# Kernel optimization log

Hardware: AMD Instinct MI355X
Metric: run time of the kernel (lower is better)

The kernel has to match this reference:

```python
import jax, jax.numpy as jnp
import numpy as np
from jax import lax

C, K, G = 256, 3, 8
CG = C // G          # group channels
P = K * K            # sampling points per group
STRIDE, PAD, DIL = 1, 1, 1
OFFSET_SCALE = 1.0
EPS = 1e-5


def setup_inputs() -> dict:
    key = jax.random.key(0)
    ks = jax.random.split(key, 8)
    N, H, W = 4, 64, 64
    return {
        "x": jax.random.normal(ks[0], (N, C, H, W), jnp.float32),
        "dw_w": jax.random.normal(ks[1], (C, 1, K, K), jnp.float32) * 0.1,
        "dw_b": jax.random.normal(ks[2], (C,), jnp.float32) * 0.01,
        "gn_g": jnp.ones((C,), jnp.float32),
        "gn_b": jnp.zeros((C,), jnp.float32),
        "off_w": jax.random.normal(ks[3], (C, G * P * 2), jnp.float32) * 0.01,
        "off_b": jax.random.normal(ks[4], (G * P * 2,), jnp.float32) * 0.1,
        "mask_w": jax.random.normal(ks[5], (C, G * P), jnp.float32) * 0.02,
        "mask_b": jax.random.normal(ks[6], (G * P,), jnp.float32) * 0.02,
    }


def _dcnv3_core(x_nhwc, offset, mask):
    # x_nhwc (N,H,W,C); offset (N,Ho,Wo,G*P*2); mask (N,Ho,Wo,G*P) already softmaxed
    inp = jnp.pad(x_nhwc, ((0, 0), (PAD, PAD), (PAD, PAD), (0, 0)))
    N, Hp, Wp, _ = inp.shape
    Ho = (Hp - (DIL * (K - 1) + 1)) // STRIDE + 1
    Wo = (Wp - (DIL * (K - 1) + 1)) // STRIDE + 1
    base = (DIL * (K - 1)) // 2 + 0.5
    ref_y = (base + jnp.arange(Ho, dtype=jnp.float32) * STRIDE) / Hp  # (Ho,)
    ref_x = (base + jnp.arange(Wo, dtype=jnp.float32) * STRIDE) / Wp  # (Wo,)
    # dilation grid; flatten order p = iw*K + ih (matches torch meshgrid(x,y) ij)
    kvals = jnp.arange(K, dtype=jnp.float32) * DIL - (DIL * (K - 1)) // 2
    gx = jnp.repeat(kvals, K) / Wp  # (P,)
    gy = jnp.tile(kvals, K) / Hp    # (P,)
    off = offset.reshape(N, Ho, Wo, G, P, 2)
    # normalized sampling locations in [0,1] (then grid_sample convention 2*loc-1)
    loc_x = ref_x[None, None, :, None, None] + gx * OFFSET_SCALE + off[..., 0] * OFFSET_SCALE / Wp
    loc_y = ref_y[None, :, None, None, None] + gy * OFFSET_SCALE + off[..., 1] * OFFSET_SCALE / Hp
    # pixel coords, align_corners=False: px = loc*size - 0.5
    px = loc_x * Wp - 0.5
    py = loc_y * Hp - 0.5
    x0 = jnp.floor(px)
    y0 = jnp.floor(py)
    wx = px - x0
    wy = py - y0
    x0i = x0.astype(jnp.int32)
    y0i = y0.astype(jnp.int32)

    inp_flat = inp.reshape(N, Hp * Wp, G, CG)
    n_idx = jnp.arange(N)[:, None, None, None, None]
    g_idx = jnp.arange(G)[None, None, None, :, None]

    def gather(yi, xi):
        # zeros padding: clamp index, zero out-of-bounds corners
        valid = (yi >= 0) & (yi < Hp) & (xi >= 0) & (xi < Wp)
        idx = jnp.clip(yi, 0, Hp - 1) * Wp + jnp.clip(xi, 0, Wp - 1)
        v = inp_flat[n_idx, idx, g_idx]  # (N,Ho,Wo,G,P,CG)
        return v * valid[..., None]

    m = mask.reshape(N, Ho, Wo, G, P)
    out = jnp.zeros((N, Ho, Wo, G, CG), jnp.float32)
    for dy, dx, w in ((0, 0, (1 - wy) * (1 - wx)), (0, 1, (1 - wy) * wx),
                      (1, 0, wy * (1 - wx)), (1, 1, wy * wx)):
        v = gather(y0i + dy, x0i + dx)
        out = out + jnp.einsum('nhwgp,nhwgpc->nhwgc', m * w, v)
    return out.reshape(N, Ho, Wo, G * CG)


def reference(x, dw_w, dw_b, gn_g, gn_b, off_w, off_b, mask_w, mask_b):
    N, _, H, W = x.shape
    # depthwise 3x3 conv (groups=channels)
    x1 = lax.conv_general_dilated(
        x, dw_w, (1, 1), [((K - 1) // 2, (K - 1) // 2)] * 2,
        dimension_numbers=('NCHW', 'OIHW', 'NCHW'), feature_group_count=C)
    x1 = x1 + dw_b[None, :, None, None]
    # GroupNorm with num_groups=1: normalize over (C,H,W) per sample
    mu = jnp.mean(x1, axis=(1, 2, 3), keepdims=True)
    var = jnp.mean((x1 - mu) ** 2, axis=(1, 2, 3), keepdims=True)
    x1 = (x1 - mu) * lax.rsqrt(var + EPS)
    x1 = x1 * gn_g[None, :, None, None] + gn_b[None, :, None, None]
    x1 = jax.nn.gelu(x1, approximate=False)
    x1 = jnp.transpose(x1, (0, 2, 3, 1))  # NHWC
    offset = x1 @ off_w + off_b                                  # (N,H,W,G*P*2)
    mask = jax.nn.softmax((x1 @ mask_w + mask_b).reshape(N, H, W, G, P), axis=-1)
    mask = mask.reshape(N, H, W, G * P)
    out = _dcnv3_core(jnp.transpose(x, (0, 2, 3, 1)), offset, mask)
    return jnp.transpose(out, (0, 3, 1, 2))  # back to NCHW
```

## Files before the change

### kernel.cpp

```cpp
#include <hip/hip_runtime.h>
#include <math.h>

#define NB   4
#define CH   256
#define HW   4096
#define NCOL 216
#define MTOT 16384
#define CHW  1048576
#define EPSV 1e-5f

#define OFF_NHWC 0
#define NHWCSZ   (NB*HW*CH/2)
#define OFF_OM   (OFF_NHWC + NHWCSZ)
#define OMSZ     (MTOT*NCOL/2)
#define OFF_AB   (OFF_OM + OMSZ)
#define ABSZ     (MTOT*CH/2)
#define OFF_WB   (OFF_AB + ABSZ)
#define WBSZ     (CH*CH/2)
#define OFF_BI   (OFF_WB + WBSZ)
#define OFF_PT   (OFF_BI + 256)

typedef short bf16x8 __attribute__((ext_vector_type(8)));
typedef float f32x4  __attribute__((ext_vector_type(4)));

__device__ __forceinline__ unsigned short f2bf(float f) {
    unsigned int u = __builtin_bit_cast(unsigned int, f);
    u += 0x7fffu + ((u >> 16) & 1u);
    return (unsigned short)(u >> 16);
}

__device__ __forceinline__ float bf2f(unsigned short s) {
    return __builtin_bit_cast(float, (unsigned int)s << 16);
}

__global__ __launch_bounds__(256) void conv_prep_kernel(
    const float* __restrict__ x, const float* __restrict__ dw_w,
    const float* __restrict__ dw_b,
    const float* __restrict__ off_w, const float* __restrict__ off_b,
    const float* __restrict__ mask_w, const float* __restrict__ mask_b,
    unsigned short* __restrict__ A, unsigned short* __restrict__ inp_nhwc,
    unsigned short* __restrict__ Wc_bt, float* __restrict__ bias,
    float* __restrict__ partials) {
    __shared__ float xs[32 * 108];
    __shared__ unsigned short tb[32 * 36];
    __shared__ float rs1[256], rs2[256];
    int b = blockIdx.x;
    int tid = threadIdx.x;
    if (b < 256) {
        int k = b, n = tid;
        float v = 0.f;
        if (n < 144)      v = off_w[k * 144 + n];
        else if (n < 216) v = mask_w[k * 72 + (n - 144)];
        Wc_bt[(size_t)n * 256 + k] = f2bf(v);
        if (b == 0) {
            float bb = 0.f;
            if (n < 144)      bb = off_b[n];
            else if (n < 216) bb = mask_b[n - 144];
            bias[n] = bb;
        }
    }
    int ct  = b & 7;
    int hwt = (b >> 3) & 127;
    int n   = b >> 10;
    int c0 = ct * 32;
    int hw0 = hwt * 32;
    int h  = hw0 >> 6;
    int w0 = hw0 & 63;
    const float* xb = x + ((size_t)n * CH + c0) * HW;
    for (int it = 0; it < 13; ++it) {
        int q = it * 256 + tid;
        if (q < 3264) {
            int cl = q / 102;
            int rr = q - cl * 102;
            int r  = rr / 34;
            int i  = rr - r * 34;
            int gh = h - 1 + r;
            int gw = w0 - 1 + i;
            float v = 0.f;
            if (gh >= 0 && gh < 64 && gw >= 0 && gw < 64)
                v = xb[(size_t)cl * HW + gh * 64 + gw];
            xs[cl * 108 + r * 36 + i] = v;
        }
    }
    __syncthreads();
    int wl = tid & 31;
    int cbase = (tid >> 5) * 4;
    float s1 = 0.f, s2 = 0.f;
    ushort4 o;
    unsigned short ov[4];
#pragma unroll
    for (int j = 0; j < 4; ++j) {
        int c = c0 + cbase + j;
        float acc = dw_b[c];
        const float* wk = dw_w + c * 9;
#pragma unroll
        for (int r = 0; r < 3; ++r)
#pragma unroll
            for (int kx = 0; kx < 3; ++kx)
                acc = fmaf(xs[(cbase + j) * 108 + r * 36 + wl + kx], wk[r * 3 + kx], acc);
        s1 += acc; s2 += acc * acc;
        ov[j] = f2bf(acc);
    }
    o.x = ov[0]; o.y = ov[1]; o.z = ov[2]; o.w = ov[3];
    *(ushort4*)&tb[wl * 36 + cbase] = o;
    rs1[tid] = s1; rs2[tid] = s2;
    {
        int r2 = tid >> 3, cg = tid & 7;
        ushort4 rv;
        rv.x = f2bf(xs[(cg * 4 + 0) * 108 + 36 + r2 + 1]);
        rv.y = f2bf(xs[(cg * 4 + 1) * 108 + 36 + r2 + 1]);
        rv.z = f2bf(xs[(cg * 4 + 2) * 108 + 36 + r2 + 1]);
        rv.w = f2bf(xs[(cg * 4 + 3) * 108 + 36 + r2 + 1]);
        *(ushort4*)&inp_nhwc[((size_t)(n * HW + hw0 + r2)) * 256 + c0 + cg * 4] = rv;
    }
    __syncthreads();
    for (int s = 128; s > 0; s >>= 1) {
        if (tid < s) { rs1[tid] += rs1[tid + s]; rs2[tid] += rs2[tid + s]; }
        __syncthreads();
    }
    if (tid == 0) {
        partials[2 * b]     = rs1[0];
        partials[2 * b + 1] = rs2[0];
    }
    int r2 = tid >> 3, cg = tid & 7;
    ushort4 w4 = *(const ushort4*)&tb[r2 * 36 + cg * 4];
    *(ushort4*)&A[((size_t)(n * HW + hw0 + r2)) * 256 + c0 + cg * 4] = w4;
}

#define LDK 72
__global__ __launch_bounds__(512) void fused_gemm_dcn_kernel(
    const unsigned short* __restrict__ A, const unsigned short* __restrict__ Bt,
    const float* __restrict__ bias, const float* __restrict__ partials,
    const float* __restrict__ gn_g, const float* __restrict__ gn_b,
    const unsigned short* __restrict__ inp_nhwc, float* __restrict__ out) {
    __shared__ unsigned short As[64 * LDK];
    __shared__ unsigned short Bs[256 * LDK];
    __shared__ float lom[64 * 216];
    __shared__ float ot[16 * 260];
    __shared__ float red1[512], red2[512];

    int bid = blockIdx.x;
    int tile = (bid & 7) * 32 + (bid >> 3);
    int m0 = tile * 64;
    int n = m0 >> 12;
    int hwb = m0 & 4095;
    int tid = threadIdx.x, lane = tid & 63, wid = tid >> 6;

    {
        const float2* p2 = (const float2*)partials;
        float2 a = p2[n * 1024 + tid];
        float2 c = p2[n * 1024 + tid + 512];
        red1[tid] = a.x + c.x;
        red2[tid] = a.y + c.y;
    }
    __syncthreads();
    for (int s = 256; s > 0; s >>= 1) {
        if (tid < s) { red1[tid] += red1[tid + s]; red2[tid] += red2[tid + s]; }
        __syncthreads();
    }
    float mean = red1[0] * (1.f / (float)CHW);
    float var  = red2[0] * (1.f / (float)CHW) - mean * mean;
    float rsig = rsqrtf(var + EPSV);

    f32x4 acc[4][2] = {};
    for (int k0 = 0; k0 < 256; k0 += 64) {
        {
            int row = tid >> 3, kk0 = (tid & 7) * 8;
            union { uint4 u; unsigned short s[8]; } in, ou;
            in.u = *(const uint4*)&A[((size_t)(m0 + row)) * 256 + k0 + kk0];
#pragma unroll
            for (int j = 0; j < 8; ++j) {
                int ch = k0 + kk0 + j;
                float v = bf2f(in.s[j]);
                v = (v - mean) * rsig * gn_g[ch] + gn_b[ch];
                v = 0.5f * v * (1.0f + erff(v * 0.70710678118654752f));
                ou.s[j] = f2bf(v);
            }
            *(uint4*)&As[row * LDK + kk0] = ou.u;
        }
#pragma unroll
        for (int i = 0; i < 4; ++i) {
            int q = i * 512 + tid;
            int mm = q >> 3, kk = (q & 7) * 8;
            *(uint4*)&Bs[mm * LDK + kk] = *(const uint4*)&Bt[(size_t)mm * 256 + k0 + kk];
        }
        __syncthreads();
#pragma unroll
        for (int kh = 0; kh < 2; ++kh) {
            bf16x8 af[4], bfr[2];
#pragma unroll
            for (int mi = 0; mi < 4; ++mi)
                af[mi] = *(const bf16x8*)&As[(mi * 16 + (lane & 15)) * LDK + kh * 32 + (lane >> 4) * 8];
#pragma unroll
            for (int nj = 0; nj < 2; ++nj)
                bfr[nj] = *(const bf16x8*)&Bs[(wid * 32 + nj * 16 + (lane & 15)) * LDK + kh * 32 + (lane >> 4) * 8];
#pragma unroll
            for (int mi = 0; mi < 4; ++mi)
#pragma unroll
                for (int nj = 0; nj < 2; ++nj)
                    acc[mi][nj] = __builtin_amdgcn_mfma_f32_16x16x32_bf16(
                        af[mi], bfr[nj], acc[mi][nj], 0, 0, 0);
        }
        __syncthreads();
    }
#pragma unroll
    for (int nj = 0; nj < 2; ++nj) {
        int col = wid * 32 + nj * 16 + (lane & 15);
        if (col < NCOL) {
            float bcol = bias[col];
#pragma unroll
            for (int mi = 0; mi < 4; ++mi)
#pragma unroll
                for (int r = 0; r < 4; ++r) {
                    int row = mi * 16 + (lane >> 4) * 4 + r;
                    lom[row * NCOL + col] = acc[mi][nj][r] + bcol;
                }
        }
    }
    __syncthreads();

    const unsigned short* base = inp_nhwc + (size_t)n * HW * 256;
    int h = hwb >> 6;
    int half = tid >> 5;
    int l  = tid & 31;
    int g  = l >> 2;
    int ch0 = l * 8;
#pragma unroll
    for (int round = 0; round < 4; ++round) {
        int pixloc = round * 16 + half;
        int w = pixloc;
        const float* lm = &lom[pixloc * NCOL];
        float lg[9];
        float mx = -1e30f;
#pragma unroll
        for (int p = 0; p < 9; ++p) { lg[p] = lm[144 + g * 9 + p]; mx = fmaxf(mx, lg[p]); }
        float sum = 0.f;
#pragma unroll
        for (int p = 0; p < 9; ++p) { lg[p] = __expf(lg[p] - mx); sum += lg[p]; }
        float rs = 1.0f / sum;
        float acc2[8] = {};
#pragma unroll
        for (int p = 0; p < 9; ++p) {
            float ox = lm[g * 18 + p * 2];
            float oy = lm[g * 18 + p * 2 + 1];
            float px = (float)(w + (p / 3)) + ox;
            float py = (float)(h + (p % 3)) + oy;
            float xf = floorf(px), yf = floorf(py);
            float wx = px - xf, wy = py - yf;
            int x0 = (int)xf, y0 = (int)yf;
            float m = lg[p] * rs;
            float w00 = m * (1.f - wy) * (1.f - wx);
            float w01 = m * (1.f - wy) * wx;
            float w10 = m * wy * (1.f - wx);
            float w11 = m * wy * wx;
#pragma unroll
            for (int corner = 0; corner < 4; ++corner) {
                int yi = y0 + (corner >> 1);
                int xi = x0 + (corner & 1);
                float cw = (corner == 0) ? w00 : (corner == 1) ? w01 : (corner == 2) ? w10 : w11;
                bool valid = (yi >= 1) & (yi <= 64) & (xi >= 1) & (xi <= 64);
                int yc = min(max(yi, 1), 64) - 1;
                int xc = min(max(xi, 1), 64) - 1;
                bf16x8 v = *(const bf16x8*)&base[((size_t)yc * 64 + xc) * 256 + ch0];
                float f = valid ? cw : 0.f;
#pragma unroll
                for (int j = 0; j < 8; ++j)
                    acc2[j] = fmaf(f, bf2f((unsigned short)v[j]), acc2[j]);
            }
        }
        *(float4*)&ot[half * 260 + ch0]     = make_float4(acc2[0], acc2[1], acc2[2], acc2[3]);
        *(float4*)&ot[half * 260 + ch0 + 4] = make_float4(acc2[4], acc2[5], acc2[6], acc2[7]);
        __syncthreads();
        int px = tid & 15, crow = tid >> 4;
#pragma unroll
        for (int cc = 0; cc < 8; ++cc) {
            int c = cc * 32 + crow;
            out[((size_t)(n * CH + c)) * HW + hwb + round * 16 + px] = ot[px * 260 + c];
        }
        __syncthreads();
    }
}

extern "C" void kernel_launch(void* const* d_in, const int* in_sizes, int n_in,
                              void* d_out, int out_size, void* d_ws, size_t ws_size,
                              hipStream_t stream) {
    const float* x      = (const float*)d_in[0];
    const float* dw_w   = (const float*)d_in[1];
    const float* dw_b   = (const float*)d_in[2];
    const float* gn_g   = (const float*)d_in[3];
    const float* gn_b   = (const float*)d_in[4];
    const float* off_w  = (const float*)d_in[5];
    const float* off_b  = (const float*)d_in[6];
    const float* mask_w = (const float*)d_in[7];
    const float* mask_b = (const float*)d_in[8];
    float* out = (float*)d_out;

    float* ws = (float*)d_ws;
    unsigned short* inp_nhwc = (unsigned short*)(ws + OFF_NHWC);
    unsigned short* Abf   = (unsigned short*)(ws + OFF_AB);
    unsigned short* Wc_bt = (unsigned short*)(ws + OFF_WB);
    float* bias     = ws + OFF_BI;
    float* partials = ws + OFF_PT;

    conv_prep_kernel<<<4096, 256, 0, stream>>>(x, dw_w, dw_b, off_w, off_b,
                                               mask_w, mask_b, Abf, inp_nhwc,
                                               Wc_bt, bias, partials);
    fused_gemm_dcn_kernel<<<256, 512, 0, stream>>>(Abf, Wc_bt, bias, partials,
                                                   gn_g, gn_b, inp_nhwc, out);
}
```

Baseline: 140.7 us.

## Vectorize halo loads, use wave-shuffle reductions, prefetch B, double-buffer output tile

Result: faster. 128.3 us (-8.8%).

```diff
diff --git a/kernel.cpp b/kernel.cpp
--- a/kernel.cpp
+++ b/kernel.cpp
@@ -41,9 +41,9 @@
     unsigned short* __restrict__ A, unsigned short* __restrict__ inp_nhwc,
     unsigned short* __restrict__ Wc_bt, float* __restrict__ bias,
     float* __restrict__ partials) {
-    __shared__ float xs[32 * 108];
+    __shared__ float xs[32 * 120];
     __shared__ unsigned short tb[32 * 36];
-    __shared__ float rs1[256], rs2[256];
+    __shared__ float rs1[4], rs2[4];
     int b = blockIdx.x;
     int tid = threadIdx.x;
     if (b < 256) {
@@ -67,20 +67,30 @@
     int h  = hw0 >> 6;
     int w0 = hw0 & 63;
     const float* xb = x + ((size_t)n * CH + c0) * HW;
-    for (int it = 0; it < 13; ++it) {
-        int q = it * 256 + tid;
-        if (q < 3264) {
-            int cl = q / 102;
-            int rr = q - cl * 102;
-            int r  = rr / 34;
-            int i  = rr - r * 34;
-            int gh = h - 1 + r;
-            int gw = w0 - 1 + i;
-            float v = 0.f;
-            if (gh >= 0 && gh < 64 && gw >= 0 && gw < 64)
-                v = xb[(size_t)cl * HW + gh * 64 + gw];
-            xs[cl * 108 + r * 36 + i] = v;
-        }
+#pragma unroll
+    for (int it = 0; it < 3; ++it) {
+        int idx = it * 256 + tid;
+        int cl  = idx / 24;
+        int rem = idx - cl * 24;
+        int r   = rem >> 3;
+        int f4  = rem & 7;
+        int gh  = h - 1 + r;
+        float4 v = make_float4(0.f, 0.f, 0.f, 0.f);
+        if (gh >= 0 && gh < 64)
+            v = *(const float4*)&xb[(size_t)cl * HW + gh * 64 + w0 + f4 * 4];
+        *(float4*)&xs[cl * 120 + r * 40 + 4 + f4 * 4] = v;
+    }
+    if (tid < 192) {
+        int cl   = tid / 6;
+        int rem  = tid - cl * 6;
+        int r    = rem >> 1;
+        int side = rem & 1;
+        int gh   = h - 1 + r;
+        int gw   = side ? (w0 + 32) : (w0 - 1);
+        float v = 0.f;
+        if (gh >= 0 && gh < 64 && gw >= 0 && gw < 64)
+            v = xb[(size_t)cl * HW + gh * 64 + gw];
+        xs[cl * 120 + r * 40 + (side ? 36 : 3)] = v;
     }
     __syncthreads();
     int wl = tid & 31;
@@ -97,30 +107,31 @@
         for (int r = 0; r < 3; ++r)
 #pragma unroll
             for (int kx = 0; kx < 3; ++kx)
-                acc = fmaf(xs[(cbase + j) * 108 + r * 36 + wl + kx], wk[r * 3 + kx], acc);
+                acc = fmaf(xs[(cbase + j) * 120 + r * 40 + wl + kx + 3], wk[r * 3 + kx], acc);
         s1 += acc; s2 += acc * acc;
         ov[j] = f2bf(acc);
     }
     o.x = ov[0]; o.y = ov[1]; o.z = ov[2]; o.w = ov[3];
     *(ushort4*)&tb[wl * 36 + cbase] = o;
-    rs1[tid] = s1; rs2[tid] = s2;
+#pragma unroll
+    for (int off = 32; off >= 1; off >>= 1) {
+        s1 += __shfl_xor(s1, off, 64);
+        s2 += __shfl_xor(s2, off, 64);
+    }
+    if ((tid & 63) == 0) { rs1[tid >> 6] = s1; rs2[tid >> 6] = s2; }
     {
         int r2 = tid >> 3, cg = tid & 7;
         ushort4 rv;
-        rv.x = f2bf(xs[(cg * 4 + 0) * 108 + 36 + r2 + 1]);
-        rv.y = f2bf(xs[(cg * 4 + 1) * 108 + 36 + r2 + 1]);
-        rv.z = f2bf(xs[(cg * 4 + 2) * 108 + 36 + r2 + 1]);
-        rv.w = f2bf(xs[(cg * 4 + 3) * 108 + 36 + r2 + 1]);
+        rv.x = f2bf(xs[(cg * 4 + 0) * 120 + 40 + r2 + 4]);
+        rv.y = f2bf(xs[(cg * 4 + 1) * 120 + 40 + r2 + 4]);
+        rv.z = f2bf(xs[(cg * 4 + 2) * 120 + 40 + r2 + 4]);
+        rv.w = f2bf(xs[(cg * 4 + 3) * 120 + 40 + r2 + 4]);
         *(ushort4*)&inp_nhwc[((size_t)(n * HW + hw0 + r2)) * 256 + c0 + cg * 4] = rv;
     }
     __syncthreads();
-    for (int s = 128; s > 0; s >>= 1) {
-        if (tid < s) { rs1[tid] += rs1[tid + s]; rs2[tid] += rs2[tid + s]; }
-        __syncthreads();
-    }
     if (tid == 0) {
-        partials[2 * b]     = rs1[0];
-        partials[2 * b + 1] = rs2[0];
+        partials[2 * b]     = rs1[0] + rs1[1] + rs1[2] + rs1[3];
+        partials[2 * b + 1] = rs2[0] + rs2[1] + rs2[2] + rs2[3];
     }
     int r2 = tid >> 3, cg = tid & 7;
     ushort4 w4 = *(const ushort4*)&tb[r2 * 36 + cg * 4];
@@ -136,8 +147,8 @@
     __shared__ unsigned short As[64 * LDK];
     __shared__ unsigned short Bs[256 * LDK];
     __shared__ float lom[64 * 216];
-    __shared__ float ot[16 * 260];
-    __shared__ float red1[512], red2[512];
+    __shared__ float ot[2 * 16 * 260];
+    __shared__ float red1[8], red2[8];
 
     int bid = blockIdx.x;
     int tile = (bid & 7) * 32 + (bid >> 3);
@@ -146,20 +157,31 @@
     int hwb = m0 & 4095;
     int tid = threadIdx.x, lane = tid & 63, wid = tid >> 6;
 
+#pragma unroll
+    for (int i = 0; i < 4; ++i) {
+        int q = i * 512 + tid;
+        int mm = q >> 3, kk = (q & 7) * 8;
+        *(uint4*)&Bs[mm * LDK + kk] = *(const uint4*)&Bt[(size_t)mm * 256 + kk];
+    }
+
     {
         const float2* p2 = (const float2*)partials;
         float2 a = p2[n * 1024 + tid];
         float2 c = p2[n * 1024 + tid + 512];
-        red1[tid] = a.x + c.x;
-        red2[tid] = a.y + c.y;
+        float s1 = a.x + c.x, s2 = a.y + c.y;
+#pragma unroll
+        for (int off = 32; off >= 1; off >>= 1) {
+            s1 += __shfl_xor(s1, off, 64);
+            s2 += __shfl_xor(s2, off, 64);
+        }
+        if (lane == 0) { red1[wid] = s1; red2[wid] = s2; }
     }
     __syncthreads();
-    for (int s = 256; s > 0; s >>= 1) {
-        if (tid < s) { red1[tid] += red1[tid + s]; red2[tid] += red2[tid + s]; }
-        __syncthreads();
-    }
-    float mean = red1[0] * (1.f / (float)CHW);
-    float var  = red2[0] * (1.f / (float)CHW) - mean * mean;
+    float t1 = 0.f, t2 = 0.f;
+#pragma unroll
+    for (int i = 0; i < 8; ++i) { t1 += red1[i]; t2 += red2[i]; }
+    float mean = t1 * (1.f / (float)CHW);
+    float var  = t2 * (1.f / (float)CHW) - mean * mean;
     float rsig = rsqrtf(var + EPSV);
 
     f32x4 acc[4][2] = {};
@@ -178,11 +200,13 @@
             }
             *(uint4*)&As[row * LDK + kk0] = ou.u;
         }
-#pragma unroll
-        for (int i = 0; i < 4; ++i) {
-            int q = i * 512 + tid;
-            int mm = q >> 3, kk = (q & 7) * 8;
-            *(uint4*)&Bs[mm * LDK + kk] = *(const uint4*)&Bt[(size_t)mm * 256 + k0 + kk];
+        if (k0) {
+#pragma unroll
+            for (int i = 0; i < 4; ++i) {
+                int q = i * 512 + tid;
+                int mm = q >> 3, kk = (q & 7) * 8;
+                *(uint4*)&Bs[mm * LDK + kk] = *(const uint4*)&Bt[(size_t)mm * 256 + k0 + kk];
+            }
         }
         __syncthreads();
 #pragma unroll
@@ -227,6 +251,7 @@
     int ch0 = l * 8;
 #pragma unroll
     for (int round = 0; round < 4; ++round) {
+        float* otb = &ot[(round & 1) * 16 * 260];
         int pixloc = round * 16 + half;
         int w = pixloc;
         const float* lm = &lom[pixloc * NCOL];
@@ -268,16 +293,15 @@
                     acc2[j] = fmaf(f, bf2f((unsigned short)v[j]), acc2[j]);
             }
         }
-        *(float4*)&ot[half * 260 + ch0]     = make_float4(acc2[0], acc2[1], acc2[2], acc2[3]);
-        *(float4*)&ot[half * 260 + ch0 + 4] = make_float4(acc2[4], acc2[5], acc2[6], acc2[7]);
+        *(float4*)&otb[half * 260 + ch0]     = make_float4(acc2[0], acc2[1], acc2[2], acc2[3]);
+        *(float4*)&otb[half * 260 + ch0 + 4] = make_float4(acc2[4], acc2[5], acc2[6], acc2[7]);
         __syncthreads();
         int px = tid & 15, crow = tid >> 4;
 #pragma unroll
         for (int cc = 0; cc < 8; ++cc) {
             int c = cc * 32 + crow;
-            out[((size_t)(n * CH + c)) * HW + hwb + round * 16 + px] = ot[px * 260 + c];
-        }
-        __syncthreads();
+            out[((size_t)(n * CH + c)) * HW + hwb + round * 16 + px] = otb[px * 260 + c];
+        }
     }
 }
 
```
